# Optimization experiments

Hardware: AMD Instinct MI355X
Metric: run time of the kernel (lower is better)

Reference implementation:

```python
import jax, jax.numpy as jnp
import numpy as np

N = 100_000   # nodes
E = 1_600_000 # edges
IN = 128      # in_feats
H = 64        # h_feats
C = 16        # num_classes
L = 4         # num_layers
EPS = 1e-5    # BatchNorm eps


def setup_inputs() -> dict:
    key = jax.random.key(0)
    ks = jax.random.split(key, 16)
    w = lambda k, shape: jax.random.normal(k, shape, dtype=jnp.float32) * 0.02
    return {
        "features": jax.random.normal(ks[0], (N, IN), dtype=jnp.float32),
        "src": jax.random.randint(ks[1], (E,), 0, N),
        "dst": jax.random.randint(ks[2], (E,), 0, N),
        # RelationPatternEncoder: Linear(IN,IN/2) ReLU Linear(IN/2,IN/4) ReLU Linear(IN/4,IN)
        "enc_W1": w(ks[3], (IN, IN // 2)), "enc_b1": jnp.zeros((IN // 2,), jnp.float32),
        "enc_W2": w(ks[4], (IN // 2, IN // 4)), "enc_b2": jnp.zeros((IN // 4,), jnp.float32),
        "enc_W3": w(ks[5], (IN // 4, IN)), "enc_b3": jnp.zeros((IN,), jnp.float32),
        # attention gate: Linear(2H,H) ReLU Linear(H,1) Sigmoid
        "att_W1": w(ks[6], (2 * H, H)), "att_b1": jnp.zeros((H,), jnp.float32),
        "att_W2": w(ks[7], (H, 1)), "att_b2": jnp.zeros((1,), jnp.float32),
        # GraphConv weights: layer 0 (IN,H); layers 1..3 (H,H) stacked
        "W0": w(ks[8], (IN, H)), "b0": jnp.zeros((H,), jnp.float32),
        "W_rest": w(ks[9], (L - 1, H, H)), "b_rest": jnp.zeros((L - 1, H), jnp.float32),
        # BatchNorm affine params per layer
        "gamma": jnp.ones((L, H), jnp.float32), "beta": jnp.zeros((L, H), jnp.float32),
        # final classifier
        "fc_W": w(ks[10], (H, C)), "fc_b": jnp.zeros((C,), jnp.float32),
    }


def reference(features, src, dst, enc_W1, enc_b1, enc_W2, enc_b2, enc_W3, enc_b3,
              att_W1, att_b1, att_W2, att_b2, W0, b0, W_rest, b_rest,
              gamma, beta, fc_W, fc_b):
    n = features.shape[0]
    ones = jnp.ones(src.shape[0], jnp.float32)
    # degrees (DGL GraphConv norm='both' clamps degrees to min 1)
    out_deg = jnp.clip(jax.ops.segment_sum(ones, src, num_segments=n), 1.0)
    in_deg = jnp.clip(jax.ops.segment_sum(ones, dst, num_segments=n), 1.0)
    out_norm = out_deg ** -0.5  # [N]
    in_norm = in_deg ** -0.5    # [N]

    def graph_conv(h, W, b):
        # symmetric-normalized SpMM: D_in^{-1/2} A^T D_out^{-1/2} h, then linear
        hs = h * out_norm[:, None]
        agg = jax.ops.segment_sum(hs[src], dst, num_segments=n)  # [N,H]
        agg = agg * in_norm[:, None]
        return agg @ W + b

    def neighbor_mean(h):
        # update_all(copy_u, mean): mean over incoming edges, 0 for isolated nodes
        s = jax.ops.segment_sum(h[src], dst, num_segments=n)
        return s / in_deg[:, None]

    def batchnorm(x, g, bta):
        mu = x.mean(axis=0)
        var = x.var(axis=0)  # biased, as PyTorch uses in training normalization
        return (x - mu) * jax.lax.rsqrt(var + EPS) * g + bta

    # relation pattern encoder (last Linear has no activation)
    h = jax.nn.relu(features @ enc_W1 + enc_b1)
    h = jax.nn.relu(h @ enc_W2 + enc_b2)
    h = h @ enc_W3 + enc_b3  # [N, IN]

    for i in range(L):
        if i >= 1:
            nb = neighbor_mean(h)                       # [N,H]
            comb = jnp.concatenate([h, nb], axis=1)     # [N,2H]
            a = jax.nn.sigmoid(jax.nn.relu(comb @ att_W1 + att_b1) @ att_W2 + att_b2)  # [N,1]
            h = h + a * nb
        W, b = (W0, b0) if i == 0 else (W_rest[i - 1], b_rest[i - 1])
        h_new = batchnorm(graph_conv(h, W, b), gamma[i], beta[i])
        if i > 0:
            h_new = h_new + h  # residual
        h = jax.nn.relu(h_new)
        # dropout: identity in eval mode

    return h @ fc_W + fc_b  # [N, C]
```

## Files before the change

### kernel.cpp

```cpp
#include <hip/hip_runtime.h>
#include <hip/hip_bf16.h>
#include <math.h>


#define EPS_BN 1e-5f

static inline int cdiv_i(int a, int b){ return (a + b - 1) / b; }

typedef __attribute__((ext_vector_type(8))) short bf16x8;
typedef __attribute__((ext_vector_type(4))) float f32x4;

__device__ inline short f2bf(float f){
  unsigned int u = __builtin_bit_cast(unsigned int, f);
  u += 0x7FFFu + ((u >> 16) & 1u);
  return (short)(u >> 16);
}
__device__ inline float bf2f(unsigned short u){
  unsigned int x = ((unsigned int)u) << 16;
  return __builtin_bit_cast(float, x);
}

__device__ inline void pack_w_lds(const float* __restrict__ W, short* WP, int K, int N){
  int NF = N >> 4;
  int items = (K >> 5) * NF * 64;
  for (int i = threadIdx.x; i < items; i += 256){
    int c  = i & 15;
    int kg = (i >> 4) & 3;
    int t2 = i >> 6;
    int nf = t2 % NF, kstep = t2 / NF;
    short* d = &WP[((kstep * NF + nf) * 4 + kg) * 128 + c * 8];
#pragma unroll
    for (int j = 0; j < 8; ++j){
      int k = kstep * 32 + kg * 8 + j;
      d[j] = f2bf(W[(size_t)k * N + nf * 16 + c]);
    }
  }
}
__device__ inline bf16x8 wfrag(const short* WP, int NF, int kstep, int nf, int lgrp, int lrow){
  return *reinterpret_cast<const bf16x8*>(&WP[((kstep * NF + nf) * 4 + lgrp) * 128 + lrow * 8]);
}

__global__ void k_cnt2(const int* __restrict__ src, const int* __restrict__ dst,
                       float* __restrict__ outd, int* __restrict__ cnt,
                       int* __restrict__ rank, int E){
  int base = blockIdx.x * (blockDim.x * 4) + threadIdx.x;
#pragma unroll
  for (int j = 0; j < 4; ++j){
    int e = base + j * 256;
    if (e < E){
      atomicAdd(&outd[src[e]], 1.f);
      rank[e] = atomicAdd(&cnt[dst[e]], 1);
    }
  }
}

__global__ void k_norm2(float* __restrict__ outn, const int* __restrict__ cnt,
                        float* __restrict__ innorm, float* __restrict__ invind, int n){
  int i = blockIdx.x * blockDim.x + threadIdx.x;
  if (i < n){
    float od = fmaxf(outn[i], 1.f);
    float id = fmaxf((float)cnt[i], 1.f);
    outn[i]   = rsqrtf(od);
    innorm[i] = rsqrtf(id);
    invind[i] = 1.f / id;
  }
}

#define SCAN_B 256
__global__ void k_scan_a(const int* __restrict__ cnt, int* __restrict__ bsum, int n){
  __shared__ int sm[SCAN_B];
  int i = blockIdx.x * SCAN_B + threadIdx.x;
  sm[threadIdx.x] = (i < n) ? cnt[i] : 0;
  __syncthreads();
  for (int s = SCAN_B / 2; s; s >>= 1){
    if (threadIdx.x < s) sm[threadIdx.x] += sm[threadIdx.x + s];
    __syncthreads();
  }
  if (threadIdx.x == 0) bsum[blockIdx.x] = sm[0];
}

__global__ void k_scan_b(int* __restrict__ bsum, int nb, int* __restrict__ rowptr_n, int E){
  __shared__ int sm[512];
  int t = threadIdx.x;
  int orig = (t < nb) ? bsum[t] : 0;
  sm[t] = orig;
  __syncthreads();
  for (int off = 1; off < 512; off <<= 1){
    int v = (t >= off) ? sm[t - off] : 0;
    __syncthreads();
    sm[t] += v;
    __syncthreads();
  }
  if (t < nb) bsum[t] = sm[t] - orig;
  if (t == 0) *rowptr_n = E;
}

__global__ void k_scan_c(const int* __restrict__ cnt, const int* __restrict__ bsum,
                         int* __restrict__ rowptr, int n){
  __shared__ int sm[SCAN_B];
  int i = blockIdx.x * SCAN_B + threadIdx.x;
  int orig = (i < n) ? cnt[i] : 0;
  sm[threadIdx.x] = orig;
  __syncthreads();
  for (int off = 1; off < SCAN_B; off <<= 1){
    int v = (threadIdx.x >= off) ? sm[threadIdx.x - off] : 0;
    __syncthreads();
    sm[threadIdx.x] += v;
    __syncthreads();
  }
  if (i < n) rowptr[i] = sm[threadIdx.x] - orig + bsum[blockIdx.x];
}

__global__ void k_fill2(const int* __restrict__ src, const int* __restrict__ dst,
                        const int* __restrict__ rowptr, const int* __restrict__ rank,
                        int* __restrict__ csr, int E){
  int base = blockIdx.x * (blockDim.x * 4) + threadIdx.x;
#pragma unroll
  for (int j = 0; j < 4; ++j){
    int e = base + j * 256;
    if (e < E) csr[rowptr[dst[e]] + rank[e]] = src[e];
  }
}

__global__ __launch_bounds__(256) void k_enc(
    const float* __restrict__ features,
    const float* __restrict__ W1, const float* __restrict__ b1,
    const float* __restrict__ W2, const float* __restrict__ b2,
    const float* __restrict__ W3, const float* __restrict__ b3,
    const float* __restrict__ W0, const float* __restrict__ outnorm,
    unsigned short* __restrict__ hw_bf, int n)
{
  __shared__ short WP1[8192];
  __shared__ short WP2[2048];
  __shared__ short WP3[4096];
  __shared__ short stA[9216];
  __shared__ short st2[2560];

  const int tid = threadIdx.x, wave = tid >> 6, lane = tid & 63;
  const int lrow = lane & 15, lgrp = lane >> 4;
  const int row0 = blockIdx.x * 64;
  const int arow = row0 + wave * 16 + lrow;
  const bool rok = arow < n;

  pack_w_lds(W1, WP1, 128, 64);
  pack_w_lds(W2, WP2, 64, 32);
  pack_w_lds(W3, WP3, 32, 128);
  __syncthreads();

  {
    f32x4 acc[4] = {};
#pragma unroll
    for (int kstep = 0; kstep < 4; ++kstep){
      bf16x8 a;
      if (rok){
        const float* p = features + (size_t)arow * 128 + kstep * 32 + lgrp * 8;
        float4 v0 = *reinterpret_cast<const float4*>(p);
        float4 v1 = *reinterpret_cast<const float4*>(p + 4);
        a[0]=f2bf(v0.x); a[1]=f2bf(v0.y); a[2]=f2bf(v0.z); a[3]=f2bf(v0.w);
        a[4]=f2bf(v1.x); a[5]=f2bf(v1.y); a[6]=f2bf(v1.z); a[7]=f2bf(v1.w);
      } else {
#pragma unroll
        for (int j = 0; j < 8; ++j) a[j] = 0;
      }
#pragma unroll
      for (int nf = 0; nf < 4; ++nf)
        acc[nf] = __builtin_amdgcn_mfma_f32_16x16x32_bf16(a, wfrag(WP1,4,kstep,nf,lgrp,lrow), acc[nf], 0,0,0);
    }
#pragma unroll
    for (int nf = 0; nf < 4; ++nf){
      float bv = b1[nf * 16 + lrow];
#pragma unroll
      for (int r = 0; r < 4; ++r)
        stA[(wave*16 + lgrp*4 + r) * 72 + nf*16 + lrow] = f2bf(fmaxf(acc[nf][r] + bv, 0.f));
    }
  }
  __syncthreads();

  pack_w_lds(W0, WP1, 128, 64);

  {
    f32x4 acc[2] = {};
#pragma unroll
    for (int kstep = 0; kstep < 2; ++kstep){
      bf16x8 a = *reinterpret_cast<const bf16x8*>(&stA[(wave*16 + lrow) * 72 + kstep*32 + lgrp*8]);
#pragma unroll
      for (int nf = 0; nf < 2; ++nf)
        acc[nf] = __builtin_amdgcn_mfma_f32_16x16x32_bf16(a, wfrag(WP2,2,kstep,nf,lgrp,lrow), acc[nf], 0,0,0);
    }
#pragma unroll
    for (int nf = 0; nf < 2; ++nf){
      float bv = b2[nf * 16 + lrow];
#pragma unroll
      for (int r = 0; r < 4; ++r)
        st2[(wave*16 + lgrp*4 + r) * 40 + nf*16 + lrow] = f2bf(fmaxf(acc[nf][r] + bv, 0.f));
    }
  }
  __syncthreads();

  {
    f32x4 acc[8] = {};
    bf16x8 a = *reinterpret_cast<const bf16x8*>(&st2[(wave*16 + lrow) * 40 + lgrp*8]);
#pragma unroll
    for (int nf = 0; nf < 8; ++nf)
      acc[nf] = __builtin_amdgcn_mfma_f32_16x16x32_bf16(a, wfrag(WP3,8,0,nf,lgrp,lrow), acc[nf], 0,0,0);
    __syncthreads();
#pragma unroll
    for (int nf = 0; nf < 8; ++nf){
      float bv = b3[nf * 16 + lrow];
#pragma unroll
      for (int r = 0; r < 4; ++r)
        stA[(wave*16 + lgrp*4 + r) * 136 + nf*16 + lrow] = f2bf(acc[nf][r] + bv);
    }
  }
  __syncthreads();

  {
    const float rs = rok ? outnorm[arow] : 0.f;
    f32x4 acc[4] = {};
#pragma unroll
    for (int kstep = 0; kstep < 4; ++kstep){
      bf16x8 raw = *reinterpret_cast<const bf16x8*>(&stA[(wave*16 + lrow) * 136 + kstep*32 + lgrp*8]);
      bf16x8 a;
#pragma unroll
      for (int j = 0; j < 8; ++j) a[j] = f2bf(bf2f((unsigned short)raw[j]) * rs);
#pragma unroll
      for (int nf = 0; nf < 4; ++nf)
        acc[nf] = __builtin_amdgcn_mfma_f32_16x16x32_bf16(a, wfrag(WP1,4,kstep,nf,lgrp,lrow), acc[nf], 0,0,0);
    }
#pragma unroll
    for (int nf = 0; nf < 4; ++nf){
#pragma unroll
      for (int r = 0; r < 4; ++r){
        int orow = row0 + wave*16 + lgrp*4 + r;
        if (orow < n) hw_bf[(size_t)orow * 64 + nf*16 + lrow] = (unsigned short)f2bf(acc[nf][r]);
      }
    }
  }
}

__global__ __launch_bounds__(256) void k_attconv(
    float* __restrict__ h, const unsigned short* __restrict__ nb_bf,
    const float* __restrict__ invind, const float* __restrict__ outnorm,
    const float* __restrict__ W1, const float* __restrict__ b1,
    const float* __restrict__ W2, const float* __restrict__ b2,
    const float* __restrict__ Wi, unsigned short* __restrict__ hw_bf, int n)
{
  __shared__ short WPA[8192];
  __shared__ short WPC[4096];
  __shared__ short ht[64 * 72];

  const int tid = threadIdx.x, wave = tid >> 6, lane = tid & 63;
  const int lrow = lane & 15, lgrp = lane >> 4;
  const int row0 = blockIdx.x * 64;
  const int arow = row0 + wave * 16 + lrow;
  const bool rok = arow < n;

  pack_w_lds(W1, WPA, 128, 64);
  pack_w_lds(Wi, WPC, 64, 64);
  __syncthreads();

  const float iv = rok ? invind[arow] : 0.f;
  f32x4 acc[4];
#pragma unroll
  for (int nf = 0; nf < 4; ++nf) acc[nf] = (f32x4){0.f,0.f,0.f,0.f};

#pragma unroll
  for (int kstep = 0; kstep < 4; ++kstep){
    bf16x8 a;
    if (rok){
      if (kstep < 2){
        const float* p = h + (size_t)arow * 64 + kstep * 32 + lgrp * 8;
        float4 v0 = *reinterpret_cast<const float4*>(p);
        float4 v1 = *reinterpret_cast<const float4*>(p + 4);
        a[0]=f2bf(v0.x); a[1]=f2bf(v0.y); a[2]=f2bf(v0.z); a[3]=f2bf(v0.w);
        a[4]=f2bf(v1.x); a[5]=f2bf(v1.y); a[6]=f2bf(v1.z); a[7]=f2bf(v1.w);
      } else {
        const unsigned short* p = nb_bf + (size_t)arow * 64 + (kstep & 1) * 32 + lgrp * 8;
        bf16x8 raw = *reinterpret_cast<const bf16x8*>(p);
#pragma unroll
        for (int j = 0; j < 8; ++j) a[j] = f2bf(bf2f((unsigned short)raw[j]) * iv);
      }
    } else {
#pragma unroll
      for (int j = 0; j < 8; ++j) a[j] = 0;
    }
#pragma unroll
    for (int nf = 0; nf < 4; ++nf)
      acc[nf] = __builtin_amdgcn_mfma_f32_16x16x32_bf16(a, wfrag(WPA,4,kstep,nf,lgrp,lrow), acc[nf], 0,0,0);
  }

  const float w2l[4] = {W2[lrow], W2[16 + lrow], W2[32 + lrow], W2[48 + lrow]};
  const float b2v = b2[0];
#pragma unroll
  for (int r = 0; r < 4; ++r){
    int orow = row0 + wave*16 + lgrp*4 + r;
    float p = 0.f;
#pragma unroll
    for (int nf = 0; nf < 4; ++nf)
      p += fmaxf(acc[nf][r] + b1[nf * 16 + lrow], 0.f) * w2l[nf];
    p += __shfl_xor(p, 1); p += __shfl_xor(p, 2);
    p += __shfl_xor(p, 4); p += __shfl_xor(p, 8);
    short h0 = 0, h1v = 0, h2v = 0, h3v = 0;
    if (orow < n){
      float a = 1.f / (1.f + expf(-(p + b2v)));
      float ivr = invind[orow];
      const unsigned short* np = nb_bf + (size_t)orow * 64 + lrow * 4;
      float4 hv = *reinterpret_cast<float4*>(&h[(size_t)orow * 64 + lrow * 4]);
      hv.x += a * bf2f(np[0]) * ivr; hv.y += a * bf2f(np[1]) * ivr;
      hv.z += a * bf2f(np[2]) * ivr; hv.w += a * bf2f(np[3]) * ivr;
      *reinterpret_cast<float4*>(&h[(size_t)orow * 64 + lrow * 4]) = hv;
      h0 = f2bf(hv.x); h1v = f2bf(hv.y); h2v = f2bf(hv.z); h3v = f2bf(hv.w);
    }
    short* d = &ht[(wave*16 + lgrp*4 + r) * 72 + lrow * 4];
    d[0] = h0; d[1] = h1v; d[2] = h2v; d[3] = h3v;
  }
  __syncthreads();

  {
    const float rs = rok ? outnorm[arow] : 0.f;
    f32x4 cacc[4];
#pragma unroll
    for (int nf = 0; nf < 4; ++nf) cacc[nf] = (f32x4){0.f,0.f,0.f,0.f};
#pragma unroll
    for (int kstep = 0; kstep < 2; ++kstep){
      bf16x8 raw = *reinterpret_cast<const bf16x8*>(&ht[(wave*16 + lrow) * 72 + kstep*32 + lgrp*8]);
      bf16x8 a;
#pragma unroll
      for (int j = 0; j < 8; ++j) a[j] = f2bf(bf2f((unsigned short)raw[j]) * rs);
#pragma unroll
      for (int nf = 0; nf < 4; ++nf)
        cacc[nf] = __builtin_amdgcn_mfma_f32_16x16x32_bf16(a, wfrag(WPC,4,kstep,nf,lgrp,lrow), cacc[nf], 0,0,0);
    }
#pragma unroll
    for (int nf = 0; nf < 4; ++nf){
#pragma unroll
      for (int r = 0; r < 4; ++r){
        int orow = row0 + wave*16 + lgrp*4 + r;
        if (orow < n) hw_bf[(size_t)orow * 64 + nf*16 + lrow] = (unsigned short)f2bf(cacc[nf][r]);
      }
    }
  }
}

template<int OBF>
__global__ void k_gather(const unsigned short* __restrict__ x,
                         const int* __restrict__ rowptr, const int* __restrict__ csr,
                         void* __restrict__ outv, int n){
  int node = blockIdx.x * 4 + (threadIdx.x >> 6);
  int f = threadIdx.x & 63;
  if (node >= n) return;
  int beg = rowptr[node], end = rowptr[node + 1];
  float a0 = 0.f, a1 = 0.f, a2 = 0.f, a3 = 0.f;
  int e = beg;
  for (; e + 3 < end; e += 4){
    int s0 = csr[e], s1 = csr[e+1], s2 = csr[e+2], s3 = csr[e+3];
    a0 += bf2f(x[(size_t)s0 * 64 + f]);
    a1 += bf2f(x[(size_t)s1 * 64 + f]);
    a2 += bf2f(x[(size_t)s2 * 64 + f]);
    a3 += bf2f(x[(size_t)s3 * 64 + f]);
  }
  for (; e < end; ++e) a0 += bf2f(x[(size_t)csr[e] * 64 + f]);
  float s = (a0 + a1) + (a2 + a3);
  if (OBF) ((unsigned short*)outv)[(size_t)node * 64 + f] = (unsigned short)f2bf(s);
  else     ((float*)outv)[(size_t)node * 64 + f] = s;
}

__global__ void k_bnstats(const float* __restrict__ agg, const float* __restrict__ innorm,
                          const float* __restrict__ b, float* __restrict__ sum,
                          float* __restrict__ sumsq, int n){
  __shared__ float s1[4][64], s2[4][64];
  int f = threadIdx.x & 63, g = threadIdx.x >> 6;
  float bf = b[f];
  float a1 = 0.f, a2 = 0.f;
  for (int row = blockIdx.x * 4 + g; row < n; row += gridDim.x * 4){
    float z = agg[(size_t)row * 64 + f] * innorm[row] + bf;
    a1 += z; a2 += z * z;
  }
  s1[g][f] = a1; s2[g][f] = a2;
  __syncthreads();
  if (threadIdx.x < 64){
    atomicAdd(&sum[f],   s1[0][f] + s1[1][f] + s1[2][f] + s1[3][f]);
    atomicAdd(&sumsq[f], s2[0][f] + s2[1][f] + s2[2][f] + s2[3][f]);
  }
}

__global__ void k_post(const float* __restrict__ agg, const float* __restrict__ innorm,
                       const float* __restrict__ b, const float* __restrict__ bnsum,
                       const float* __restrict__ bnsq, const float* __restrict__ gamma,
                       const float* __restrict__ beta, float inv_n,
                       const float* __restrict__ hres,
                       float* __restrict__ hout, unsigned short* __restrict__ hbf, int n64){
  int i = blockIdx.x * blockDim.x + threadIdx.x;
  if (i >= n64) return;
  int f = i & 63, row = i >> 6;
  float mu  = bnsum[f] * inv_n;
  float var = bnsq[f] * inv_n - mu * mu;
  float sc  = gamma[f] * rsqrtf(var + EPS_BN);
  float sh  = beta[f] - mu * sc;
  float z = agg[i] * innorm[row] + b[f];
  z = z * sc + sh;
  if (hres) z += hres[i];
  float r = fmaxf(z, 0.f);
  hout[i] = r;
  hbf[i] = (unsigned short)f2bf(r);
}

__global__ __launch_bounds__(256) void k_postfc(
    const float* __restrict__ agg, const float* __restrict__ innorm,
    const float* __restrict__ b, const float* __restrict__ bnsum,
    const float* __restrict__ bnsq, const float* __restrict__ gamma,
    const float* __restrict__ beta, float inv_n,
    const float* __restrict__ hres, const float* __restrict__ fcW,
    const float* __restrict__ fcb, float* __restrict__ out, int n)
{
  __shared__ short hb[64 * 72];
  __shared__ short WPF[1024];

  const int tid = threadIdx.x, wave = tid >> 6, lane = tid & 63;
  const int lrow = lane & 15, lgrp = lane >> 4;
  const int row0 = blockIdx.x * 64;

  pack_w_lds(fcW, WPF, 64, 16);

#pragma unroll
  for (int j = 0; j < 16; ++j){
    int idx = j * 256 + tid;
    int row = idx >> 6, f = idx & 63;
    int grow = row0 + row;
    float r = 0.f;
    if (grow < n){
      float mu  = bnsum[f] * inv_n;
      float var = bnsq[f] * inv_n - mu * mu;
      float sc  = gamma[f] * rsqrtf(var + EPS_BN);
      float sh  = beta[f] - mu * sc;
      float z = agg[(size_t)grow * 64 + f] * innorm[grow] + b[f];
      z = z * sc + sh + hres[(size_t)grow * 64 + f];
      r = fmaxf(z, 0.f);
    }
    hb[row * 72 + f] = f2bf(r);
  }
  __syncthreads();

  f32x4 acc = (f32x4){0.f,0.f,0.f,0.f};
#pragma unroll
  for (int kstep = 0; kstep < 2; ++kstep){
    bf16x8 a = *reinterpret_cast<const bf16x8*>(&hb[(wave*16 + lrow) * 72 + kstep*32 + lgrp*8]);
    acc = __builtin_amdgcn_mfma_f32_16x16x32_bf16(a, wfrag(WPF,1,kstep,0,lgrp,lrow), acc, 0,0,0);
  }
  float bv = fcb[lrow];
#pragma unroll
  for (int r = 0; r < 4; ++r){
    int orow = row0 + wave*16 + lgrp*4 + r;
    if (orow < n) out[(size_t)orow * 16 + lrow] = acc[r] + bv;
  }
}

extern "C" void kernel_launch(void* const* d_in, const int* in_sizes, int n_in,
                              void* d_out, int out_size, void* d_ws, size_t ws_size,
                              hipStream_t stream) {
  const float* features = (const float*)d_in[0];
  const int*   src      = (const int*)d_in[1];
  const int*   dst      = (const int*)d_in[2];
  const float* encW1 = (const float*)d_in[3];  const float* encb1 = (const float*)d_in[4];
  const float* encW2 = (const float*)d_in[5];  const float* encb2 = (const float*)d_in[6];
  const float* encW3 = (const float*)d_in[7];  const float* encb3 = (const float*)d_in[8];
  const float* attW1 = (const float*)d_in[9];  const float* attb1 = (const float*)d_in[10];
  const float* attW2 = (const float*)d_in[11]; const float* attb2 = (const float*)d_in[12];
  const float* W0    = (const float*)d_in[13]; const float* b0    = (const float*)d_in[14];
  const float* Wrest = (const float*)d_in[15]; const float* brest = (const float*)d_in[16];
  const float* gamma = (const float*)d_in[17]; const float* beta  = (const float*)d_in[18];
  const float* fcW   = (const float*)d_in[19]; const float* fcb   = (const float*)d_in[20];
  float* out = (float*)d_out;

  const int n = in_sizes[0] / 128;
  const int E = in_sizes[1];

  float* ws      = (float*)d_ws;
  float* agg     = ws;
  unsigned short* h_bf = (unsigned short*)(ws + (size_t)n * 64);
  float* hbuf    = ws + (size_t)n * 128;
  float* nbhw    = hbuf + (size_t)n * 64;
  float* outnorm = nbhw + (size_t)n * 64;
  float* innorm  = outnorm + n;
  float* invind  = innorm + n;
  float* bnsum   = invind + n;
  float* bnsq    = bnsum + 256;
  int* cnt    = (int*)(bnsq + 256);
  int* rowptr = cnt + n;
  int* csr    = rowptr + n + 1;
  int* bsum   = csr + E;
  int* rank = (int*)nbhw;
  unsigned short* nb_bf = (unsigned short*)nbhw;
  unsigned short* hw_bf = (unsigned short*)(nbhw + (size_t)n * 32);

  const int nt = cdiv_i(n, 64);
  const int nb = cdiv_i(n, SCAN_B);
  const float inv_n = 1.f / (float)n;

  hipMemsetAsync(outnorm, 0, (size_t)n * sizeof(float), stream);
  hipMemsetAsync(cnt, 0, (size_t)n * sizeof(int), stream);
  hipMemsetAsync(bnsum, 0, 512 * sizeof(float), stream);
  k_cnt2<<<cdiv_i(E, 1024), 256, 0, stream>>>(src, dst, outnorm, cnt, rank, E);
  k_scan_a<<<nb, SCAN_B, 0, stream>>>(cnt, bsum, n);
  k_scan_b<<<1, 512, 0, stream>>>(bsum, nb, rowptr + n, E);
  k_scan_c<<<nb, SCAN_B, 0, stream>>>(cnt, bsum, rowptr, n);
  k_norm2<<<cdiv_i(n, 256), 256, 0, stream>>>(outnorm, cnt, innorm, invind, n);
  k_fill2<<<cdiv_i(E, 1024), 256, 0, stream>>>(src, dst, rowptr, rank, csr, E);

  k_enc<<<nt, 256, 0, stream>>>(features, encW1, encb1, encW2, encb2, encW3, encb3,
                                W0, outnorm, hw_bf, n);
  k_gather<0><<<cdiv_i(n, 4), 256, 0, stream>>>(hw_bf, rowptr, csr, agg, n);
  k_bnstats<<<512, 256, 0, stream>>>(agg, innorm, b0, bnsum, bnsq, n);
  k_post<<<cdiv_i(n * 64, 256), 256, 0, stream>>>(agg, innorm, b0, bnsum, bnsq, gamma, beta, inv_n,
                                                  nullptr, hbuf, h_bf, n * 64);

  for (int i = 1; i < 4; ++i){
    const float* Wi = Wrest + (size_t)(i - 1) * 64 * 64;
    const float* bi = brest + (size_t)(i - 1) * 64;
    k_gather<1><<<cdiv_i(n, 4), 256, 0, stream>>>(h_bf, rowptr, csr, nb_bf, n);
    k_attconv<<<nt, 256, 0, stream>>>(hbuf, nb_bf, invind, outnorm,
                                      attW1, attb1, attW2, attb2, Wi, hw_bf, n);
    k_gather<0><<<cdiv_i(n, 4), 256, 0, stream>>>(hw_bf, rowptr, csr, agg, n);
    k_bnstats<<<512, 256, 0, stream>>>(agg, innorm, bi, bnsum + i * 64, bnsq + i * 64, n);
    if (i < 3){
      k_post<<<cdiv_i(n * 64, 256), 256, 0, stream>>>(agg, innorm, bi, bnsum + i * 64, bnsq + i * 64,
                                                      gamma + i * 64, beta + i * 64, inv_n,
                                                      hbuf, hbuf, h_bf, n * 64);
    } else {
      k_postfc<<<nt, 256, 0, stream>>>(agg, innorm, bi, bnsum + i * 64, bnsq + i * 64,
                                       gamma + i * 64, beta + i * 64, inv_n,
                                       hbuf, fcW, fcb, out, n);
    }
  }
}
```

Before: 874.1 us.

## Fuse gather with BatchNorm stats, use deterministic partial reduction, vectorize post

The SpMM gather now also computes the BatchNorm sum and sum-of-squares partials, so the separate k_bnstats pass that re-read agg is removed. Per-block partials go to a workspace and a small reduction kernel finishes them, replacing the atomics and the bnsum memset. The degree-norm kernel is merged into the first scan kernel, two memsets are merged into one, and k_post handles four features per thread with float4 loads. The gather is now a grid-stride loop over a fixed 2048 blocks, which may change load balance and occupancy compared with one launch per node group.

Result: faster. 788.8 us (-9.8%).

```diff
diff --git a/kernel.cpp b/kernel.cpp
--- a/kernel.cpp
+++ b/kernel.cpp
@@ -4,11 +4,13 @@
 
 
 #define EPS_BN 1e-5f
+#define GS_BLOCKS 2048
 
 static inline int cdiv_i(int a, int b){ return (a + b - 1) / b; }
 
 typedef __attribute__((ext_vector_type(8))) short bf16x8;
 typedef __attribute__((ext_vector_type(4))) float f32x4;
+typedef __attribute__((ext_vector_type(4))) unsigned short u16x4;
 
 __device__ inline short f2bf(float f){
   unsigned int u = __builtin_bit_cast(unsigned int, f);
@@ -54,23 +56,21 @@
   }
 }
 
-__global__ void k_norm2(float* __restrict__ outn, const int* __restrict__ cnt,
-                        float* __restrict__ innorm, float* __restrict__ invind, int n){
-  int i = blockIdx.x * blockDim.x + threadIdx.x;
+#define SCAN_B 256
+__global__ void k_scan_a(const int* __restrict__ cnt, int* __restrict__ bsum,
+                         float* __restrict__ outn, float* __restrict__ innorm,
+                         float* __restrict__ invind, int n){
+  __shared__ int sm[SCAN_B];
+  int i = blockIdx.x * SCAN_B + threadIdx.x;
+  int c = (i < n) ? cnt[i] : 0;
   if (i < n){
     float od = fmaxf(outn[i], 1.f);
-    float id = fmaxf((float)cnt[i], 1.f);
+    float id = fmaxf((float)c, 1.f);
     outn[i]   = rsqrtf(od);
     innorm[i] = rsqrtf(id);
     invind[i] = 1.f / id;
   }
-}
-
-#define SCAN_B 256
-__global__ void k_scan_a(const int* __restrict__ cnt, int* __restrict__ bsum, int n){
-  __shared__ int sm[SCAN_B];
-  int i = blockIdx.x * SCAN_B + threadIdx.x;
-  sm[threadIdx.x] = (i < n) ? cnt[i] : 0;
+  sm[threadIdx.x] = c;
   __syncthreads();
   for (int s = SCAN_B / 2; s; s >>= 1){
     if (threadIdx.x < s) sm[threadIdx.x] += sm[threadIdx.x + s];
@@ -342,10 +342,9 @@
   }
 }
 
-template<int OBF>
-__global__ void k_gather(const unsigned short* __restrict__ x,
-                         const int* __restrict__ rowptr, const int* __restrict__ csr,
-                         void* __restrict__ outv, int n){
+__global__ void k_gather_nb(const unsigned short* __restrict__ x,
+                            const int* __restrict__ rowptr, const int* __restrict__ csr,
+                            unsigned short* __restrict__ outv, int n){
   int node = blockIdx.x * 4 + (threadIdx.x >> 6);
   int f = threadIdx.x & 63;
   if (node >= n) return;
@@ -360,28 +359,57 @@
     a3 += bf2f(x[(size_t)s3 * 64 + f]);
   }
   for (; e < end; ++e) a0 += bf2f(x[(size_t)csr[e] * 64 + f]);
-  float s = (a0 + a1) + (a2 + a3);
-  if (OBF) ((unsigned short*)outv)[(size_t)node * 64 + f] = (unsigned short)f2bf(s);
-  else     ((float*)outv)[(size_t)node * 64 + f] = s;
-}
-
-__global__ void k_bnstats(const float* __restrict__ agg, const float* __restrict__ innorm,
-                          const float* __restrict__ b, float* __restrict__ sum,
-                          float* __restrict__ sumsq, int n){
+  outv[(size_t)node * 64 + f] = (unsigned short)f2bf((a0 + a1) + (a2 + a3));
+}
+
+__global__ __launch_bounds__(256) void k_gather_stats(
+    const unsigned short* __restrict__ x, const int* __restrict__ rowptr,
+    const int* __restrict__ csr, const float* __restrict__ innorm,
+    const float* __restrict__ b, float* __restrict__ agg,
+    float* __restrict__ p1, float* __restrict__ p2, int n){
   __shared__ float s1[4][64], s2[4][64];
-  int f = threadIdx.x & 63, g = threadIdx.x >> 6;
+  int g = threadIdx.x >> 6, f = threadIdx.x & 63;
   float bf = b[f];
-  float a1 = 0.f, a2 = 0.f;
-  for (int row = blockIdx.x * 4 + g; row < n; row += gridDim.x * 4){
-    float z = agg[(size_t)row * 64 + f] * innorm[row] + bf;
-    a1 += z; a2 += z * z;
-  }
-  s1[g][f] = a1; s2[g][f] = a2;
+  float z1 = 0.f, z2 = 0.f;
+  for (int node = blockIdx.x * 4 + g; node < n; node += GS_BLOCKS * 4){
+    int beg = rowptr[node], end = rowptr[node + 1];
+    float a0 = 0.f, a1 = 0.f, a2 = 0.f, a3 = 0.f;
+    int e = beg;
+    for (; e + 3 < end; e += 4){
+      int s0v = csr[e], s1v = csr[e+1], s2v = csr[e+2], s3v = csr[e+3];
+      a0 += bf2f(x[(size_t)s0v * 64 + f]);
+      a1 += bf2f(x[(size_t)s1v * 64 + f]);
+      a2 += bf2f(x[(size_t)s2v * 64 + f]);
+      a3 += bf2f(x[(size_t)s3v * 64 + f]);
+    }
+    for (; e < end; ++e) a0 += bf2f(x[(size_t)csr[e] * 64 + f]);
+    float s = (a0 + a1) + (a2 + a3);
+    agg[(size_t)node * 64 + f] = s;
+    float z = s * innorm[node] + bf;
+    z1 += z; z2 += z * z;
+  }
+  s1[g][f] = z1; s2[g][f] = z2;
   __syncthreads();
   if (threadIdx.x < 64){
-    atomicAdd(&sum[f],   s1[0][f] + s1[1][f] + s1[2][f] + s1[3][f]);
-    atomicAdd(&sumsq[f], s2[0][f] + s2[1][f] + s2[2][f] + s2[3][f]);
-  }
+    p1[(size_t)blockIdx.x * 64 + f] = s1[0][f] + s1[1][f] + s1[2][f] + s1[3][f];
+    p2[(size_t)blockIdx.x * 64 + f] = s2[0][f] + s2[1][f] + s2[2][f] + s2[3][f];
+  }
+}
+
+__global__ void k_bnred(const float* __restrict__ p1, const float* __restrict__ p2,
+                        float* __restrict__ bnsum, float* __restrict__ bnsq){
+  __shared__ float sm[256];
+  int f = blockIdx.x & 63, stat = blockIdx.x >> 6;
+  const float* p = stat ? p2 : p1;
+  float a = 0.f;
+  for (int i = threadIdx.x; i < GS_BLOCKS; i += 256) a += p[(size_t)i * 64 + f];
+  sm[threadIdx.x] = a;
+  __syncthreads();
+  for (int s = 128; s; s >>= 1){
+    if (threadIdx.x < s) sm[threadIdx.x] += sm[threadIdx.x + s];
+    __syncthreads();
+  }
+  if (threadIdx.x == 0) (stat ? bnsq : bnsum)[f] = sm[0];
 }
 
 __global__ void k_post(const float* __restrict__ agg, const float* __restrict__ innorm,
@@ -389,20 +417,31 @@
                        const float* __restrict__ bnsq, const float* __restrict__ gamma,
                        const float* __restrict__ beta, float inv_n,
                        const float* __restrict__ hres,
-                       float* __restrict__ hout, unsigned short* __restrict__ hbf, int n64){
+                       float* __restrict__ hout, unsigned short* __restrict__ hbf, int n16){
   int i = blockIdx.x * blockDim.x + threadIdx.x;
-  if (i >= n64) return;
-  int f = i & 63, row = i >> 6;
-  float mu  = bnsum[f] * inv_n;
-  float var = bnsq[f] * inv_n - mu * mu;
-  float sc  = gamma[f] * rsqrtf(var + EPS_BN);
-  float sh  = beta[f] - mu * sc;
-  float z = agg[i] * innorm[row] + b[f];
-  z = z * sc + sh;
-  if (hres) z += hres[i];
-  float r = fmaxf(z, 0.f);
-  hout[i] = r;
-  hbf[i] = (unsigned short)f2bf(r);
+  if (i >= n16) return;
+  int row = i >> 4, fq = (i & 15) * 4;
+  size_t o = (size_t)row * 64 + fq;
+  float inn = innorm[row];
+  float4 av = *reinterpret_cast<const float4*>(&agg[o]);
+  float4 rv = hres ? *reinterpret_cast<const float4*>(&hres[o]) : (float4){0.f,0.f,0.f,0.f};
+  float r[4]; float aa[4] = {av.x, av.y, av.z, av.w}; float rr[4] = {rv.x, rv.y, rv.z, rv.w};
+#pragma unroll
+  for (int j = 0; j < 4; ++j){
+    int f = fq + j;
+    float mu  = bnsum[f] * inv_n;
+    float var = bnsq[f] * inv_n - mu * mu;
+    float sc  = gamma[f] * rsqrtf(var + EPS_BN);
+    float sh  = beta[f] - mu * sc;
+    float z = aa[j] * inn + b[f];
+    z = z * sc + sh + rr[j];
+    r[j] = fmaxf(z, 0.f);
+  }
+  *reinterpret_cast<float4*>(&hout[o]) = (float4){r[0], r[1], r[2], r[3]};
+  u16x4 hb;
+#pragma unroll
+  for (int j = 0; j < 4; ++j) hb[j] = (unsigned short)f2bf(r[j]);
+  *reinterpret_cast<u16x4*>(&hbf[o]) = hb;
 }
 
 __global__ __launch_bounds__(256) void k_postfc(
@@ -478,15 +517,17 @@
   float* ws      = (float*)d_ws;
   float* agg     = ws;
   unsigned short* h_bf = (unsigned short*)(ws + (size_t)n * 64);
+  float* p1      = ws + (size_t)n * 96;
+  float* p2      = p1 + (size_t)GS_BLOCKS * 64;
   float* hbuf    = ws + (size_t)n * 128;
   float* nbhw    = hbuf + (size_t)n * 64;
   float* outnorm = nbhw + (size_t)n * 64;
-  float* innorm  = outnorm + n;
+  int*   cnt     = (int*)(outnorm + n);
+  float* innorm  = (float*)(cnt + n);
   float* invind  = innorm + n;
   float* bnsum   = invind + n;
   float* bnsq    = bnsum + 256;
-  int* cnt    = (int*)(bnsq + 256);
-  int* rowptr = cnt + n;
+  int* rowptr = (int*)(bnsq + 256);
   int* csr    = rowptr + n + 1;
   int* bsum   = csr + E;
   int* rank = (int*)nbhw;
@@ -497,35 +538,32 @@
   const int nb = cdiv_i(n, SCAN_B);
   const float inv_n = 1.f / (float)n;
 
-  hipMemsetAsync(outnorm, 0, (size_t)n * sizeof(float), stream);
-  hipMemsetAsync(cnt, 0, (size_t)n * sizeof(int), stream);
-  hipMemsetAsync(bnsum, 0, 512 * sizeof(float), stream);
+  hipMemsetAsync(outnorm, 0, 2 * (size_t)n * sizeof(float), stream);
   k_cnt2<<<cdiv_i(E, 1024), 256, 0, stream>>>(src, dst, outnorm, cnt, rank, E);
-  k_scan_a<<<nb, SCAN_B, 0, stream>>>(cnt, bsum, n);
+  k_scan_a<<<nb, SCAN_B, 0, stream>>>(cnt, bsum, outnorm, innorm, invind, n);
   k_scan_b<<<1, 512, 0, stream>>>(bsum, nb, rowptr + n, E);
   k_scan_c<<<nb, SCAN_B, 0, stream>>>(cnt, bsum, rowptr, n);
-  k_norm2<<<cdiv_i(n, 256), 256, 0, stream>>>(outnorm, cnt, innorm, invind, n);
   k_fill2<<<cdiv_i(E, 1024), 256, 0, stream>>>(src, dst, rowptr, rank, csr, E);
 
   k_enc<<<nt, 256, 0, stream>>>(features, encW1, encb1, encW2, encb2, encW3, encb3,
                                 W0, outnorm, hw_bf, n);
-  k_gather<0><<<cdiv_i(n, 4), 256, 0, stream>>>(hw_bf, rowptr, csr, agg, n);
-  k_bnstats<<<512, 256, 0, stream>>>(agg, innorm, b0, bnsum, bnsq, n);
-  k_post<<<cdiv_i(n * 64, 256), 256, 0, stream>>>(agg, innorm, b0, bnsum, bnsq, gamma, beta, inv_n,
-                                                  nullptr, hbuf, h_bf, n * 64);
+  k_gather_stats<<<GS_BLOCKS, 256, 0, stream>>>(hw_bf, rowptr, csr, innorm, b0, agg, p1, p2, n);
+  k_bnred<<<128, 256, 0, stream>>>(p1, p2, bnsum, bnsq);
+  k_post<<<cdiv_i(n * 16, 256), 256, 0, stream>>>(agg, innorm, b0, bnsum, bnsq, gamma, beta, inv_n,
+                                                  nullptr, hbuf, h_bf, n * 16);
 
   for (int i = 1; i < 4; ++i){
     const float* Wi = Wrest + (size_t)(i - 1) * 64 * 64;
     const float* bi = brest + (size_t)(i - 1) * 64;
-    k_gather<1><<<cdiv_i(n, 4), 256, 0, stream>>>(h_bf, rowptr, csr, nb_bf, n);
+    k_gather_nb<<<cdiv_i(n, 4), 256, 0, stream>>>(h_bf, rowptr, csr, nb_bf, n);
     k_attconv<<<nt, 256, 0, stream>>>(hbuf, nb_bf, invind, outnorm,
                                       attW1, attb1, attW2, attb2, Wi, hw_bf, n);
-    k_gather<0><<<cdiv_i(n, 4), 256, 0, stream>>>(hw_bf, rowptr, csr, agg, n);
-    k_bnstats<<<512, 256, 0, stream>>>(agg, innorm, bi, bnsum + i * 64, bnsq + i * 64, n);
+    k_gather_stats<<<GS_BLOCKS, 256, 0, stream>>>(hw_bf, rowptr, csr, innorm, bi, agg, p1, p2, n);
+    k_bnred<<<128, 256, 0, stream>>>(p1, p2, bnsum + i * 64, bnsq + i * 64);
     if (i < 3){
-      k_post<<<cdiv_i(n * 64, 256), 256, 0, stream>>>(agg, innorm, bi, bnsum + i * 64, bnsq + i * 64,
+      k_post<<<cdiv_i(n * 16, 256), 256, 0, stream>>>(agg, innorm, bi, bnsum + i * 64, bnsq + i * 64,
                                                       gamma + i * 64, beta + i * 64, inv_n,
-                                                      hbuf, hbuf, h_bf, n * 64);
+                                                      hbuf, hbuf, h_bf, n * 16);
     } else {
       k_postfc<<<nt, 256, 0, stream>>>(agg, innorm, bi, bnsum + i * 64, bnsq + i * 64,
                                        gamma + i * 64, beta + i * 64, inv_n,
```
